# Optimization experiments

Measured on AMD Instinct MI355X. Metric: run time of the kernel, lower is better.

## Reference

```python
import jax, jax.numpy as jnp
import numpy as np

K = 7  # kernel_size
D = 2  # dilation


def window_start(idx, L, K, D):
    """NATTEN neighborhood window start (clamped at borders, dilation-group aware)."""
    nh = K // 2
    if D <= 1:
        return jnp.maximum(idx - nh, 0) + jnp.where(idx + nh >= L, L - idx - nh - 1, 0)
    ni = idx - nh * D
    imodd = idx % D
    a = (L // D) * D
    b = L - a
    right = jnp.where(imodd < b, L - b + imodd - 2 * nh * D, a + imodd - K * D)
    return jnp.where(ni < 0, imodd, jnp.where(idx + nh * D >= L, right, ni))


def setup_inputs() -> dict:
    key = jax.random.key(0)
    ks = jax.random.split(key, 7)
    B, Cin, H, W, Cout = 2, 128, 112, 112, 64
    x = jax.random.normal(ks[0], (B, Cin, H, W), dtype=jnp.float32)
    Wq = jax.random.normal(ks[1], (Cout, Cin), dtype=jnp.float32) * 0.02
    Wk = jax.random.normal(ks[2], (Cout, Cin), dtype=jnp.float32) * 0.02
    Wv = jax.random.normal(ks[3], (Cout, Cin), dtype=jnp.float32) * 0.02
    bq = jax.random.normal(ks[4], (Cout,), dtype=jnp.float32) * 0.02
    bk = jax.random.normal(ks[5], (Cout,), dtype=jnp.float32) * 0.02
    bv = jax.random.normal(ks[6], (Cout,), dtype=jnp.float32) * 0.02
    return {"x": x, "Wq": Wq, "bq": bq, "Wk": Wk, "bk": bk, "Wv": Wv, "bv": bv}


def reference(x, Wq, bq, Wk, bk, Wv, bv):
    B, Cin, H, W = x.shape
    # 1x1 conv projections -> channels-last [B, H, W, C]
    q = jnp.einsum('bchw,oc->bhwo', x, Wq) + bq
    k = jnp.einsum('bchw,oc->bhwo', x, Wk) + bk
    v = jnp.einsum('bchw,oc->bhwo', x, Wv) + bv
    C = q.shape[-1]
    scale = jnp.asarray(C, q.dtype) ** -0.5  # NATTEN default scale (heads=1, head_dim=C)

    offs = jnp.arange(K) * D
    ih = window_start(jnp.arange(H), H, K, D)[:, None] + offs  # [H, K]
    iw = window_start(jnp.arange(W), W, K, D)[:, None] + offs  # [W, K]
    # gather neighborhoods -> [B, H, W, K, K, C]
    idx_h = ih[:, None, :, None]  # [H,1,K,1]
    idx_w = iw[None, :, None, :]  # [1,W,1,K]
    kw = k[:, idx_h, idx_w, :]
    vw = v[:, idx_h, idx_w, :]

    scores = jnp.einsum('bhwc,bhwijc->bhwij', q * scale, kw)  # [B,H,W,K,K]
    attn = jax.nn.softmax(scores.reshape(B, H, W, K * K), axis=-1)
    out = jnp.einsum('bhwn,bhwnc->bhwc', attn, vw.reshape(B, H, W, K * K, C))
    return out.transpose(0, 3, 1, 2)  # [B, C, H, W]
```

## Files before the change

kernel.cpp:

```cpp
#include <hip/hip_runtime.h>
#include <hip/hip_bf16.h>

#define HWSZ 12544
#define WDIM 112
#define CIN  128
#define NPIX 25088
#define VTROW 6272

typedef __attribute__((ext_vector_type(8))) short          short8;
typedef __attribute__((ext_vector_type(4))) float          float4v;
typedef __attribute__((ext_vector_type(4))) unsigned short ushort4v;

__device__ __forceinline__ int window_start7x2(int idx, int L) {
    int ni = idx - 6;
    int imodd = idx & 1;
    int a = (L >> 1) << 1;
    int bb = L - a;
    int right = (imodd < bb) ? (L - bb + imodd - 12) : (a + imodd - 14);
    if (ni < 0) return imodd;
    if (idx + 6 >= L) return right;
    return ni;
}

__device__ __forceinline__ unsigned short f2bf(float f) {
    __hip_bfloat16 h = __float2bfloat16(f);
    return *(unsigned short*)&h;
}

__global__ __launch_bounds__(256) void proj_mfma(
    const float* __restrict__ x,
    const float* __restrict__ Wq, const float* __restrict__ bq,
    const float* __restrict__ Wk, const float* __restrict__ bk,
    const float* __restrict__ Wv, const float* __restrict__ bv,
    unsigned short* __restrict__ qbuf)
{
    __shared__ __align__(16) unsigned short wsb[64][136];

    const int t = threadIdx.x, lane = t & 63, wv = t >> 6, quad = lane >> 4;
    const int m = blockIdx.y;
    const float* Wm = (m == 0) ? Wq : (m == 1) ? Wk : Wv;
    const float* bm = (m == 0) ? bq : (m == 1) ? bk : bv;

    const int pix0 = blockIdx.x * 64;
    const int b    = blockIdx.x / 196;
    const int hw0  = pix0 - b * HWSZ;
    const float* xb = x + (size_t)b * CIN * HWSZ;

    #pragma unroll
    for (int i = 0; i < 8; ++i) {
        int u = t + 256 * i;
        int o = u >> 5, cq = (u & 31) * 4;
        float4 w4 = *(const float4*)&Wm[o * 128 + cq];
        ushort4v s4 = { f2bf(w4.x), f2bf(w4.y), f2bf(w4.z), f2bf(w4.w) };
        *(ushort4v*)&wsb[o][cq] = s4;
    }

    const int hwpx = hw0 + wv * 16 + (lane & 15);
    short8 af[4];
    #pragma unroll
    for (int kc = 0; kc < 4; ++kc) {
        #pragma unroll
        for (int j = 0; j < 8; ++j) {
            int c = kc * 32 + quad * 8 + j;
            af[kc][j] = (short)f2bf(xb[(size_t)c * HWSZ + hwpx]);
        }
    }
    __syncthreads();

    float4v acc[4] = {{0,0,0,0},{0,0,0,0},{0,0,0,0},{0,0,0,0}};
    #pragma unroll
    for (int kc = 0; kc < 4; ++kc) {
        #pragma unroll
        for (int nt = 0; nt < 4; ++nt) {
            short8 bf = *(const short8*)&wsb[nt * 16 + (lane & 15)][kc * 32 + quad * 8];
            acc[nt] = __builtin_amdgcn_mfma_f32_16x16x32_bf16(af[kc], bf, acc[nt], 0, 0, 0);
        }
    }

    if (m < 2) {
        const float scale = (m == 0) ? 0.125f : 1.0f;
        unsigned short* outm = qbuf + (size_t)m * NPIX * 64;
        #pragma unroll
        for (int nt = 0; nt < 4; ++nt) {
            int o = nt * 16 + (lane & 15);
            float bias = bm[o];
            #pragma unroll
            for (int r = 0; r < 4; ++r) {
                int px = wv * 16 + quad * 4 + r;
                outm[(size_t)(pix0 + px) * 64 + o] = f2bf(acc[nt][r] + bias);
            }
        }
    } else {
        unsigned short* vt = qbuf + 2 * (size_t)NPIX * 64;
        #pragma unroll
        for (int nt = 0; nt < 4; ++nt) {
            int ch = nt * 16 + (lane & 15);
            float bias = bm[ch];
            #pragma unroll
            for (int r = 0; r < 4; ++r) {
                int hw = hw0 + wv * 16 + quad * 4 + r;
                int h2 = (unsigned)hw / 112u;
                int w  = hw - h2 * 112;
                vt[(size_t)((b * 2 + (w & 1)) * 64 + ch) * VTROW + h2 * 56 + (w >> 1)]
                    = f2bf(acc[nt][r] + bias);
            }
        }
    }
}

__global__ __launch_bounds__(64) void attn_mfma(
    const unsigned short* __restrict__ qkv, float* __restrict__ out)
{
    __shared__ __align__(16) unsigned short ps[16 * 232];

    const int lane = threadIdx.x, quad = lane >> 4, col = lane & 15;
    const int bx  = blockIdx.x;
    const int b   = bx / 896;  const int rem = bx - b * 896;
    const int h   = rem >> 3;  const int sub = rem & 7;
    const int g   = sub & 1;
    const int pbi = sub >> 1;
    const int pb  = (pbi < 3) ? pbi * 16 : 40;

    const int hs  = window_start7x2(h, WDIM);
    const int ws0 = window_start7x2(2 * pb + g, WDIM);
    const int cb0 = (ws0 >> 1) & ~7;
    const int pixbase = b * HWSZ;

    const unsigned short* qg = qkv;
    const unsigned short* kg = qkv + (size_t)NPIX * 64;
    const unsigned short* vt = qkv + 2 * (size_t)NPIX * 64
                             + (size_t)(b * 2 + g) * 64 * VTROW;

    const int qpix = pixbase + h * WDIM + 2 * (pb + col) + g;
    short8 af0 = *(const short8*)(qg + (size_t)qpix * 64 + quad * 8);
    short8 af1 = *(const short8*)(qg + (size_t)qpix * 64 + 32 + quad * 8);

    int cbr[4];
    #pragma unroll
    for (int r = 0; r < 4; ++r)
        cbr[r] = (window_start7x2(2 * (pb + quad * 4 + r) + g, WDIM) >> 1) - cb0;

    float4v S[14];
    #pragma unroll
    for (int nt = 0; nt < 14; ++nt) {
        int u = nt * 16 + col;
        int i = u >> 5, c = u & 31;
        int wcol = cb0 + c;
        int kw = 2 * wcol + g; kw = (kw > 111) ? 111 : kw;
        int kp = pixbase + (hs + 2 * i) * WDIM + kw;
        float4v a = {0, 0, 0, 0};
        a = __builtin_amdgcn_mfma_f32_16x16x32_bf16(
                af0, *(const short8*)(kg + (size_t)kp * 64 + quad * 8), a, 0, 0, 0);
        a = __builtin_amdgcn_mfma_f32_16x16x32_bf16(
                af1, *(const short8*)(kg + (size_t)kp * 64 + 32 + quad * 8), a, 0, 0, 0);
        bool colok = (wcol <= 55);
        #pragma unroll
        for (int r = 0; r < 4; ++r) {
            bool valid = colok && ((unsigned)(c - cbr[r]) < 7u);
            S[nt][r] = valid ? a[r] * 0.125f : -1e30f;
        }
    }

    #pragma unroll
    for (int r = 0; r < 4; ++r) {
        float mx = S[0][r];
        #pragma unroll
        for (int nt = 1; nt < 14; ++nt) mx = fmaxf(mx, S[nt][r]);
        #pragma unroll
        for (int msk = 1; msk < 16; msk <<= 1)
            mx = fmaxf(mx, __shfl_xor(mx, msk, 64));
        float sum = 0.0f;
        #pragma unroll
        for (int nt = 0; nt < 14; ++nt) {
            float e = __expf(S[nt][r] - mx);
            S[nt][r] = e;
            sum += e;
        }
        #pragma unroll
        for (int msk = 1; msk < 16; msk <<= 1)
            sum += __shfl_xor(sum, msk, 64);
        float rinv = 1.0f / sum;
        int row = quad * 4 + r;
        #pragma unroll
        for (int nt = 0; nt < 14; ++nt)
            ps[row * 232 + nt * 16 + col] = f2bf(S[nt][r] * rinv);
    }

    float4v O[4] = {{0,0,0,0},{0,0,0,0},{0,0,0,0},{0,0,0,0}};
    #pragma unroll
    for (int kc = 0; kc < 7; ++kc) {
        short8 pa = *(const short8*)&ps[col * 232 + kc * 32 + quad * 8];
        int u8 = kc * 32 + quad * 8;
        int i = u8 >> 5, c0 = u8 & 31;
        int rowoff = (hs + 2 * i) * 56 + cb0 + c0;
        #pragma unroll
        for (int nt = 0; nt < 4; ++nt) {
            short8 vb = *(const short8*)(vt + (size_t)(nt * 16 + col) * VTROW + rowoff);
            O[nt] = __builtin_amdgcn_mfma_f32_16x16x32_bf16(pa, vb, O[nt], 0, 0, 0);
        }
    }

    #pragma unroll
    for (int nt = 0; nt < 4; ++nt) {
        int ch = nt * 16 + col;
        float* ob = out + (size_t)(b * 64 + ch) * HWSZ + h * WDIM;
        #pragma unroll
        for (int r = 0; r < 4; ++r)
            ob[2 * (pb + quad * 4 + r) + g] = O[nt][r];
    }
}

extern "C" void kernel_launch(void* const* d_in, const int* in_sizes, int n_in,
                              void* d_out, int out_size, void* d_ws, size_t ws_size,
                              hipStream_t stream) {
    const float* x  = (const float*)d_in[0];
    const float* Wq = (const float*)d_in[1];
    const float* bq = (const float*)d_in[2];
    const float* Wk = (const float*)d_in[3];
    const float* bk = (const float*)d_in[4];
    const float* Wv = (const float*)d_in[5];
    const float* bv = (const float*)d_in[6];
    float* out = (float*)d_out;

    unsigned short* qkv = (unsigned short*)d_ws;

    proj_mfma<<<dim3(392, 3), dim3(256), 0, stream>>>(x, Wq, bq, Wk, bk, Wv, bv, qkv);
    attn_mfma<<<dim3(1792), dim3(64), 0, stream>>>(qkv, out);
}
```

Measured before the change: 99.90 us.

## Stage projection outputs through LDS for coalesced stores; prefetch first V tile

The projection kernel now writes its bias-added bf16 results into a shared-memory transpose buffer and then emits 16-byte vector stores per thread, replacing scattered 2-byte global stores for both the Q/K layout and the parity-split V layout. The attention kernel precomputes V row offsets and issues the first V-tile loads before the QK/softmax phase so their latency overlaps compute. This adds extra LDS traffic, two barriers and more registers in exchange for fewer uncoalesced global writes.

```diff
diff --git a/kernel.cpp b/kernel.cpp
--- a/kernel.cpp
+++ b/kernel.cpp
@@ -35,8 +35,10 @@
     unsigned short* __restrict__ qbuf)
 {
     __shared__ __align__(16) unsigned short wsb[64][136];
+    __shared__ __align__(16) unsigned short trans[64 * 80];
 
     const int t = threadIdx.x, lane = t & 63, wv = t >> 6, quad = lane >> 4;
+    const int col = lane & 15;
     const int m = blockIdx.y;
     const float* Wm = (m == 0) ? Wq : (m == 1) ? Wk : Wv;
     const float* bm = (m == 0) ? bq : (m == 1) ? bk : bv;
@@ -55,7 +57,7 @@
         *(ushort4v*)&wsb[o][cq] = s4;
     }
 
-    const int hwpx = hw0 + wv * 16 + (lane & 15);
+    const int hwpx = hw0 + wv * 16 + col;
     short8 af[4];
     #pragma unroll
     for (int kc = 0; kc < 4; ++kc) {
@@ -72,39 +74,48 @@
     for (int kc = 0; kc < 4; ++kc) {
         #pragma unroll
         for (int nt = 0; nt < 4; ++nt) {
-            short8 bf = *(const short8*)&wsb[nt * 16 + (lane & 15)][kc * 32 + quad * 8];
+            short8 bf = *(const short8*)&wsb[nt * 16 + col][kc * 32 + quad * 8];
             acc[nt] = __builtin_amdgcn_mfma_f32_16x16x32_bf16(af[kc], bf, acc[nt], 0, 0, 0);
         }
     }
+    __syncthreads();
 
     if (m < 2) {
-        const float scale = (m == 0) ? 0.125f : 1.0f;
-        unsigned short* outm = qbuf + (size_t)m * NPIX * 64;
-        #pragma unroll
-        for (int nt = 0; nt < 4; ++nt) {
-            int o = nt * 16 + (lane & 15);
-            float bias = bm[o];
+        #pragma unroll
+        for (int nt = 0; nt < 4; ++nt) {
+            float bias = bm[nt * 16 + col];
             #pragma unroll
             for (int r = 0; r < 4; ++r) {
                 int px = wv * 16 + quad * 4 + r;
-                outm[(size_t)(pix0 + px) * 64 + o] = f2bf(acc[nt][r] + bias);
+                trans[px * 80 + nt * 16 + col] = f2bf(acc[nt][r] + bias);
             }
         }
+        __syncthreads();
+        unsigned short* outm = qbuf + (size_t)m * NPIX * 64;
+        const int tpx = t >> 2, chunk = t & 3;
+        const unsigned short* src = &trans[tpx * 80 + chunk * 16];
+        unsigned short* dst = outm + (size_t)(pix0 + tpx) * 64 + chunk * 16;
+        *(short8*)(dst)     = *(const short8*)(src);
+        *(short8*)(dst + 8) = *(const short8*)(src + 8);
     } else {
-        unsigned short* vt = qbuf + 2 * (size_t)NPIX * 64;
-        #pragma unroll
-        for (int nt = 0; nt < 4; ++nt) {
-            int ch = nt * 16 + (lane & 15);
+        #pragma unroll
+        for (int nt = 0; nt < 4; ++nt) {
+            int ch = nt * 16 + col;
             float bias = bm[ch];
             #pragma unroll
             for (int r = 0; r < 4; ++r) {
-                int hw = hw0 + wv * 16 + quad * 4 + r;
-                int h2 = (unsigned)hw / 112u;
-                int w  = hw - h2 * 112;
-                vt[(size_t)((b * 2 + (w & 1)) * 64 + ch) * VTROW + h2 * 56 + (w >> 1)]
-                    = f2bf(acc[nt][r] + bias);
+                int px = wv * 16 + quad * 4 + r;
+                trans[ch * 80 + (px & 1) * 40 + (px >> 1)] = f2bf(acc[nt][r] + bias);
             }
         }
+        __syncthreads();
+        unsigned short* vt = qbuf + 2 * (size_t)NPIX * 64;
+        const int ch = t >> 2, parity = (t >> 1) & 1, half = t & 1;
+        const unsigned short* src = &trans[ch * 80 + parity * 40 + half * 16];
+        unsigned short* dst = vt + (size_t)((b * 2 + parity) * 64 + ch) * VTROW
+                            + (hw0 >> 1) + half * 16;
+        *(short8*)(dst)     = *(const short8*)(src);
+        *(short8*)(dst + 8) = *(const short8*)(src + 8);
     }
 }
 
@@ -139,6 +150,17 @@
     #pragma unroll
     for (int r = 0; r < 4; ++r)
         cbr[r] = (window_start7x2(2 * (pb + quad * 4 + r) + g, WDIM) >> 1) - cb0;
+
+    int rowoff[7];
+    #pragma unroll
+    for (int kc = 0; kc < 7; ++kc) {
+        int u8 = kc * 32 + quad * 8;
+        rowoff[kc] = (hs + 2 * (u8 >> 5)) * 56 + cb0 + (u8 & 31);
+    }
+    short8 vb0[4];
+    #pragma unroll
+    for (int nt = 0; nt < 4; ++nt)
+        vb0[nt] = *(const short8*)(vt + (size_t)(nt * 16 + col) * VTROW + rowoff[0]);
 
     float4v S[14];
     #pragma unroll
@@ -187,15 +209,18 @@
     }
 
     float4v O[4] = {{0,0,0,0},{0,0,0,0},{0,0,0,0},{0,0,0,0}};
-    #pragma unroll
-    for (int kc = 0; kc < 7; ++kc) {
+    {
+        short8 pa = *(const short8*)&ps[col * 232 + quad * 8];
+        #pragma unroll
+        for (int nt = 0; nt < 4; ++nt)
+            O[nt] = __builtin_amdgcn_mfma_f32_16x16x32_bf16(pa, vb0[nt], O[nt], 0, 0, 0);
+    }
+    #pragma unroll
+    for (int kc = 1; kc < 7; ++kc) {
         short8 pa = *(const short8*)&ps[col * 232 + kc * 32 + quad * 8];
-        int u8 = kc * 32 + quad * 8;
-        int i = u8 >> 5, c0 = u8 & 31;
-        int rowoff = (hs + 2 * i) * 56 + cb0 + c0;
-        #pragma unroll
-        for (int nt = 0; nt < 4; ++nt) {
-            short8 vb = *(const short8*)(vt + (size_t)(nt * 16 + col) * VTROW + rowoff);
+        #pragma unroll
+        for (int nt = 0; nt < 4; ++nt) {
+            short8 vb = *(const short8*)(vt + (size_t)(nt * 16 + col) * VTROW + rowoff[kc]);
             O[nt] = __builtin_amdgcn_mfma_f32_16x16x32_bf16(pa, vb, O[nt], 0, 0, 0);
         }
     }
```

New measurement: 98.36 us. Within noise of the previous version (-1.5%).
